# Optimization experiments

Measured on AMD Instinct MI355X. Metric: run time of the kernel, lower is better.

## Reference

```python
import jax, jax.numpy as jnp
import numpy as np

NUM_HEADS = 16


def setup_inputs() -> dict:
    key = jax.random.key(0)
    k1, k2, k3 = jax.random.split(key, 3)
    B, S, D = 4, 2048, 1024
    hidden_states = jax.random.normal(k1, (B, S, D), dtype=jnp.float32)
    w_qkv = jax.random.normal(k2, (D, 3 * D), dtype=jnp.float32) * (1.0 / np.sqrt(D))
    w_out = jax.random.normal(k3, (D, D), dtype=jnp.float32) * (1.0 / np.sqrt(D))
    return {"hidden_states": hidden_states, "w_qkv": w_qkv, "w_out": w_out}


def reference(hidden_states, w_qkv, w_out):
    B, S, D = hidden_states.shape
    H = NUM_HEADS
    d = D // H
    # fused QKV projection: [B, S, 3D] -> [3, B, S, H, d]
    qkv = (hidden_states @ w_qkv).reshape(B, S, 3, H, d)
    q, k, v = jnp.moveaxis(qkv, 2, 0)  # each [B, S, H, d]
    scale = 1.0 / np.sqrt(d).astype(np.float32)
    scores = jnp.einsum("bqhd,bkhd->bhqk", q, k) * scale  # [B, H, S, S]
    attn = jax.nn.softmax(scores, axis=-1)
    ctx = jnp.einsum("bhqk,bkhd->bqhd", attn, v).reshape(B, S, D)
    return ctx @ w_out
```

## Files before the change

kernel.cpp:

```cpp
#include <hip/hip_runtime.h>
#include <hip/hip_bf16.h>
#include <math.h>

typedef __bf16 bf16;
typedef __bf16 bf16x4 __attribute__((ext_vector_type(4)));
typedef __bf16 bf16x8 __attribute__((ext_vector_type(8)));
typedef float  f32x4  __attribute__((ext_vector_type(4)));

#define B_  4
#define S_  2048
#define D_  1024
#define H_  16
#define DH  64
#define M_  (B_*S_)
#define BH_ (B_*H_)

#define QSCALE 0.18033688011112042f

__device__ __forceinline__ void glds16(const bf16* g, bf16* l) {
  __builtin_amdgcn_global_load_lds((const __attribute__((address_space(1))) void*)g,
                                   (__attribute__((address_space(3))) void*)l, 16, 0, 0);
}

__global__ __launch_bounds__(256) void prep(const float* __restrict__ hidden, bf16* __restrict__ hb,
                                            const float* __restrict__ wqkv, const float* __restrict__ wout,
                                            bf16* __restrict__ wqkvT, bf16* __restrict__ woutT) {
  int bx = blockIdx.x, tid = threadIdx.x;
  if (bx < 8192) {
    int i = (bx * 256 + tid) * 4;
    float4 v = *(const float4*)(hidden + i);
    bf16x4 o = { (bf16)v.x, (bf16)v.y, (bf16)v.z, (bf16)v.w };
    *(bf16x4*)(hb + i) = o;
    return;
  }
  __shared__ float tile[32][33];
  int t = bx - 8192;
  const float* in; bf16* out; int C, c0, r0;
  if (t < 96 * 32) { in = wqkv; out = wqkvT; C = 3072; c0 = (t % 96) * 32; r0 = (t / 96) * 32; }
  else { t -= 96 * 32;  in = wout; out = woutT; C = 1024; c0 = (t % 32) * 32; r0 = (t / 32) * 32; }
  int tx = tid & 31, ty = tid >> 5;
  #pragma unroll
  for (int i = ty; i < 32; i += 8) tile[i][tx] = in[(size_t)(r0 + i) * C + c0 + tx];
  __syncthreads();
  #pragma unroll
  for (int i = ty; i < 32; i += 8) out[(size_t)(c0 + i) * D_ + r0 + tx] = (bf16)tile[tx][i];
}

#define BM 256
#define BN 128
#define BK 64
#define NTILE (D_ / BK)
#define ATILE (BM * BK)
#define BTILE (BN * BK)

__device__ __forceinline__ void core256(const bf16* __restrict__ A, const bf16* __restrict__ Bt,
                                        int m0, int n0, bf16* As, bf16* Bs, int tid,
                                        f32x4 acc[4][4]) {
  const int wave = tid >> 6, lane = tid & 63, quad = lane >> 4, l16 = lane & 15;
  const int wm = (wave >> 1) * 64, wn = (wave & 1) * 64;
  const int lr8 = lane >> 3, lg = lane & 7;
  const int sg = ((lg ^ lr8) << 3);
  const bf16* gA = A  + (size_t)(m0 + lr8) * D_ + sg;
  const bf16* gB = Bt + (size_t)(n0 + lr8) * D_ + sg;
  const int swq  = ((quad ^ (l16 & 7)) << 3);
  const int swq4 = (((4 + quad) ^ (l16 & 7)) << 3);

#define STAGE256(slot, kt) do {                                                    \
    int koff = (kt) * BK;                                                          \
    bf16* a_d = As + (slot) * ATILE + wave * 2048;                                 \
    bf16* b_d = Bs + (slot) * BTILE + wave * 1024;                                 \
    _Pragma("unroll")                                                              \
    for (int i_ = 0; i_ < 4; i_++)                                                 \
      glds16(gA + (size_t)(wave * 32 + i_ * 8) * D_ + koff, a_d + i_ * 512);       \
    _Pragma("unroll")                                                              \
    for (int i_ = 0; i_ < 2; i_++)                                                 \
      glds16(gB + (size_t)(wave * 16 + i_ * 8) * D_ + koff, b_d + i_ * 512);       \
  } while (0)

#define RDFRAG(slot, sw, af, bfr) do {                                             \
    const bf16* a_s = As + (slot) * ATILE;                                         \
    const bf16* b_s = Bs + (slot) * BTILE;                                         \
    _Pragma("unroll")                                                              \
    for (int i_ = 0; i_ < 4; i_++) af[i_]  = *(const bf16x8*)(a_s + (wm + i_ * 16 + l16) * 64 + (sw)); \
    _Pragma("unroll")                                                              \
    for (int j_ = 0; j_ < 4; j_++) bfr[j_] = *(const bf16x8*)(b_s + (wn + j_ * 16 + l16) * 64 + (sw)); \
  } while (0)

#define MFMA16(af, bfr) do {                                                       \
    __builtin_amdgcn_s_setprio(1);                                                 \
    _Pragma("unroll")                                                              \
    for (int i_ = 0; i_ < 4; i_++)                                                 \
      _Pragma("unroll")                                                            \
      for (int j_ = 0; j_ < 4; j_++)                                               \
        acc[i_][j_] = __builtin_amdgcn_mfma_f32_16x16x32_bf16(af[i_], bfr[j_], acc[i_][j_], 0, 0, 0); \
    __builtin_amdgcn_s_setprio(0);                                                 \
  } while (0)

  STAGE256(0, 0); STAGE256(1, 1);
  asm volatile("s_waitcnt vmcnt(6)" ::: "memory");
  __builtin_amdgcn_sched_barrier(0);
  __builtin_amdgcn_s_barrier();
  __builtin_amdgcn_sched_barrier(0);

  int scur = 0, snxt = 2;
  for (int t = 0; t < NTILE; t++) {
    bf16x8 afA[4], bfA[4];
    RDFRAG(scur, swq, afA, bfA);
    if (t + 2 < NTILE) STAGE256(snxt, t + 2);
    __builtin_amdgcn_sched_barrier(0);
    __builtin_amdgcn_s_barrier();
    __builtin_amdgcn_sched_barrier(0);
    MFMA16(afA, bfA);
    bf16x8 afB[4], bfB[4];
    RDFRAG(scur, swq4, afB, bfB);
    MFMA16(afB, bfB);
    __builtin_amdgcn_sched_barrier(0);
    if (t < NTILE - 2)       asm volatile("s_waitcnt vmcnt(6)" ::: "memory");
    else if (t == NTILE - 2) asm volatile("s_waitcnt vmcnt(0)" ::: "memory");
    __builtin_amdgcn_sched_barrier(0);
    if (t < NTILE - 1) {
      __builtin_amdgcn_s_barrier();
      __builtin_amdgcn_sched_barrier(0);
    }
    scur = (scur == 2) ? 0 : scur + 1;
    snxt = (snxt == 2) ? 0 : snxt + 1;
  }
#undef STAGE256
#undef RDFRAG
#undef MFMA16
}

__global__ __launch_bounds__(512, 1) void gemm_qkv(const bf16* __restrict__ A, const bf16* __restrict__ Bt,
                                                   bf16* __restrict__ Qb, bf16* __restrict__ Kb,
                                                   bf16* __restrict__ Vtb) {
  __shared__ __attribute__((aligned(16))) bf16 As[3 * ATILE];
  __shared__ __attribute__((aligned(16))) bf16 Bs[3 * BTILE];
  int tid = threadIdx.x;
  int m0 = blockIdx.y * BM, n0 = blockIdx.x * BN;
  f32x4 acc[4][4] = {};
  core256(A, Bt, m0, n0, As, Bs, tid, acc);
  int wave = tid >> 6, lane = tid & 63, quad = lane >> 4, l16 = lane & 15;
  int wm = (wave >> 1) * 64, wn = (wave & 1) * 64;
  int which = n0 >> 10;
  if (which == 2) {
    #pragma unroll
    for (int i = 0; i < 4; i++) {
      int mb = m0 + wm + i * 16 + quad * 4;
      int b = mb >> 11, s = mb & 2047;
      #pragma unroll
      for (int j = 0; j < 4; j++) {
        int n = n0 + wn + j * 16 + l16;
        int h = (n >> 6) & 15, dd = n & 63;
        bf16x4 v4 = { (bf16)acc[i][j][0], (bf16)acc[i][j][1], (bf16)acc[i][j][2], (bf16)acc[i][j][3] };
        *(bf16x4*)(Vtb + ((size_t)(b * H_ + h) * DH + dd) * S_ + s) = v4;
      }
    }
  } else {
    bf16* dst = (which == 0) ? Qb : Kb;
    float sc = (which == 0) ? QSCALE : 1.0f;
    #pragma unroll
    for (int i = 0; i < 4; i++) {
      #pragma unroll
      for (int j = 0; j < 4; j++) {
        int n = n0 + wn + j * 16 + l16;
        int h = (n >> 6) & 15, dd = n & 63;
        #pragma unroll
        for (int r = 0; r < 4; r++) {
          int m = m0 + wm + i * 16 + quad * 4 + r;
          int b = m >> 11, s = m & 2047;
          dst[(((size_t)(b * H_ + h)) * S_ + s) * DH + dd] = (bf16)(acc[i][j][r] * sc);
        }
      }
    }
  }
}

__global__ __launch_bounds__(512, 1) void gemm_out(const bf16* __restrict__ A, const bf16* __restrict__ Bt,
                                                   float* __restrict__ C) {
  __shared__ __attribute__((aligned(16))) bf16 As[3 * ATILE];
  __shared__ __attribute__((aligned(16))) bf16 Bs[3 * BTILE];
  int tid = threadIdx.x;
  int m0 = blockIdx.x * BM, n0 = blockIdx.y * BN;
  f32x4 acc[4][4] = {};
  core256(A, Bt, m0, n0, As, Bs, tid, acc);
  int wave = tid >> 6, lane = tid & 63, quad = lane >> 4, l16 = lane & 15;
  int wm = (wave >> 1) * 64, wn = (wave & 1) * 64;
  #pragma unroll
  for (int i = 0; i < 4; i++)
    #pragma unroll
    for (int j = 0; j < 4; j++) {
      int n = n0 + wn + j * 16 + l16;
      #pragma unroll
      for (int r = 0; r < 4; r++) {
        int m = m0 + wm + i * 16 + quad * 4 + r;
        C[(size_t)m * D_ + n] = acc[i][j][r];
      }
    }
}

#define NT  (S_ / 64)

#define KVSW(row, col) (((row) * 64) + ((col) ^ (((row) & 7) << 3)))
#define PSW(row, col)  (((row) * 32) + ((col) ^ ((((row) >> 1) & 3) << 3)))

__global__ __launch_bounds__(256, 2) void attn(const bf16* __restrict__ Qb, const bf16* __restrict__ Kb,
                                               const bf16* __restrict__ Vtb, bf16* __restrict__ ctx) {
  __shared__ __attribute__((aligned(16))) bf16 Ks[2][64 * 64];
  __shared__ __attribute__((aligned(16))) bf16 Vs[2][64 * 64];
  __shared__ __attribute__((aligned(16))) bf16 Ps[4][64 * 32];
  int tid = threadIdx.x;
  int wave = tid >> 6, lane = tid & 63, quad = lane >> 4, l16 = lane & 15;
  int bh = blockIdx.x;
  int b = bh >> 4, h = bh & 15;
  int q0 = blockIdx.y * 256 + wave * 64;
  const bf16* Qp = Qb  + (size_t)bh * S_ * DH;
  const bf16* Kp = Kb  + (size_t)bh * S_ * DH;
  const bf16* Vp = Vtb + (size_t)bh * DH * S_;

  int srow = tid >> 3, scc = (tid & 7) << 3;
  int swz = KVSW(srow, scc);

  bf16x8 qf[4][2];
  #pragma unroll
  for (int nq = 0; nq < 4; nq++)
    #pragma unroll
    for (int ks = 0; ks < 2; ks++)
      qf[nq][ks] = *(const bf16x8*)(Qp + (size_t)(q0 + nq * 16 + l16) * DH + ks * 32 + quad * 8);

  bf16 one1 = (bf16)1.0f;
  bf16x8 onesf = { one1, one1, one1, one1, one1, one1, one1, one1 };

  f32x4 o[4][4] = {};
  f32x4 oden[4] = {};

  {
    bf16x8 k0a = *(const bf16x8*)(Kp + (size_t)srow * DH + scc);
    bf16x8 k0b = *(const bf16x8*)(Kp + (size_t)(32 + srow) * DH + scc);
    bf16x8 v0a = *(const bf16x8*)(Vp + (size_t)srow * S_ + scc);
    bf16x8 v0b = *(const bf16x8*)(Vp + (size_t)(32 + srow) * S_ + scc);
    *(bf16x8*)(Ks[0] + swz)             = k0a;
    *(bf16x8*)(Ks[0] + swz + 32 * 64)   = k0b;
    *(bf16x8*)(Vs[0] + swz)             = v0a;
    *(bf16x8*)(Vs[0] + swz + 32 * 64)   = v0b;
  }

  for (int kt = 0; kt < NT; kt++) {
    int cur = kt & 1;
    __syncthreads();

    bf16x8 ka, kb2, va, vb;
    if (kt + 1 < NT) {
      const bf16* Kn = Kp + (size_t)(kt + 1) * 64 * DH;
      const bf16* Vn = Vp + (size_t)(kt + 1) * 64;
      ka  = *(const bf16x8*)(Kn + (size_t)srow * DH + scc);
      kb2 = *(const bf16x8*)(Kn + (size_t)(32 + srow) * DH + scc);
      va  = *(const bf16x8*)(Vn + (size_t)srow * S_ + scc);
      vb  = *(const bf16x8*)(Vn + (size_t)(32 + srow) * S_ + scc);
    }

    bf16x8 vf[4][2];
    #pragma unroll
    for (int td = 0; td < 4; td++)
      #pragma unroll
      for (int ks = 0; ks < 2; ks++)
        vf[td][ks] = *(const bf16x8*)(Vs[cur] + KVSW(td * 16 + l16, ks * 32 + quad * 8));

    #pragma unroll
    for (int hh = 0; hh < 2; hh++) {
      #pragma unroll
      for (int kq2 = 0; kq2 < 2; kq2++) {
        int kq = hh * 2 + kq2;
        bf16x8 kfr[2];
        #pragma unroll
        for (int ks = 0; ks < 2; ks++)
          kfr[ks] = *(const bf16x8*)(Ks[cur] + KVSW(kq * 16 + l16, ks * 32 + quad * 8));
        #pragma unroll
        for (int nq = 0; nq < 4; nq++) {
          f32x4 st = {};
          st = __builtin_amdgcn_mfma_f32_16x16x32_bf16(kfr[0], qf[nq][0], st, 0, 0, 0);
          st = __builtin_amdgcn_mfma_f32_16x16x32_bf16(kfr[1], qf[nq][1], st, 0, 0, 0);
          bf16x4 pk;
          #pragma unroll
          for (int r = 0; r < 4; r++) pk[r] = (bf16)__builtin_amdgcn_exp2f(st[r]);
          *(bf16x4*)(&Ps[wave][PSW(nq * 16 + l16, kq2 * 16 + quad * 4)]) = pk;
        }
      }
      #pragma unroll
      for (int nq = 0; nq < 4; nq++) {
        bf16x8 pf = *(const bf16x8*)(&Ps[wave][PSW(nq * 16 + l16, quad * 8)]);
        oden[nq] = __builtin_amdgcn_mfma_f32_16x16x32_bf16(pf, onesf, oden[nq], 0, 0, 0);
        #pragma unroll
        for (int td = 0; td < 4; td++)
          o[nq][td] = __builtin_amdgcn_mfma_f32_16x16x32_bf16(pf, vf[td][hh], o[nq][td], 0, 0, 0);
      }
    }

    if (kt + 1 < NT) {
      int nxt = cur ^ 1;
      *(bf16x8*)(Ks[nxt] + swz)           = ka;
      *(bf16x8*)(Ks[nxt] + swz + 32 * 64) = kb2;
      *(bf16x8*)(Vs[nxt] + swz)           = va;
      *(bf16x8*)(Vs[nxt] + swz + 32 * 64) = vb;
    }
  }

  #pragma unroll
  for (int nq = 0; nq < 4; nq++) {
    #pragma unroll
    for (int r = 0; r < 4; r++) {
      float inv = 1.0f / oden[nq][r];
      int q = q0 + nq * 16 + quad * 4 + r;
      #pragma unroll
      for (int td = 0; td < 4; td++) {
        int dd = td * 16 + l16;
        ctx[((size_t)(b * S_) + q) * D_ + h * DH + dd] = (bf16)(o[nq][td][r] * inv);
      }
    }
  }
}

extern "C" void kernel_launch(void* const* d_in, const int* in_sizes, int n_in,
                              void* d_out, int out_size, void* d_ws, size_t ws_size,
                              hipStream_t stream) {
  (void)in_sizes; (void)n_in; (void)out_size; (void)ws_size;
  const float* hidden = (const float*)d_in[0];
  const float* w_qkv  = (const float*)d_in[1];
  const float* w_out  = (const float*)d_in[2];
  float* out = (float*)d_out;

  char* ws = (char*)d_ws;
  size_t off = 0;
  bf16* hb    = (bf16*)(ws + off); off += (size_t)M_ * D_ * 2;
  bf16* wqkvT = (bf16*)(ws + off); off += (size_t)3 * D_ * D_ * 2;
  bf16* woutT = (bf16*)(ws + off); off += (size_t)D_ * D_ * 2;
  bf16* Qb    = (bf16*)(ws + off); off += (size_t)M_ * D_ * 2;
  bf16* Kb    = (bf16*)(ws + off); off += (size_t)M_ * D_ * 2;
  bf16* Vtb   = (bf16*)(ws + off); off += (size_t)M_ * D_ * 2;
  bf16* ctxb  = hb;

  prep<<<8192 + 96 * 32 + 32 * 32, 256, 0, stream>>>(hidden, hb, w_qkv, w_out, wqkvT, woutT);
  gemm_qkv<<<dim3(3 * D_ / BN, M_ / BM), 512, 0, stream>>>(hb, wqkvT, Qb, Kb, Vtb);
  attn<<<dim3(BH_, S_ / 256), 256, 0, stream>>>(Qb, Kb, Vtb, ctxb);
  gemm_out<<<dim3(M_ / BM, D_ / BN), 512, 0, stream>>>(ctxb, woutT, out);
}
```

Before: 253.8 us.

## Split GEMM K-tile into two barrier-separated phases with interleaved half-stage loads

Restructures the GEMM main loop so each K-tile runs as two phases. Each phase reads its LDS fragments, issues half of the next tile's global-to-LDS loads, hits a barrier, then runs 16 MFMAs. The last two tiles are peeled out of the loop so the waitcnt conditionals disappear. The aim is to spread global loads and LDS reads more evenly across MFMA bursts and keep waves in lockstep. The cost is an extra barrier and an explicit lgkmcnt(0) wait per phase.

```diff
diff --git a/kernel.cpp b/kernel.cpp
--- a/kernel.cpp
+++ b/kernel.cpp
@@ -65,16 +65,22 @@
   const int swq  = ((quad ^ (l16 & 7)) << 3);
   const int swq4 = (((4 + quad) ^ (l16 & 7)) << 3);
 
-#define STAGE256(slot, kt) do {                                                    \
+#define STAGE_H1(slot, kt) do {                                                    \
     int koff = (kt) * BK;                                                          \
     bf16* a_d = As + (slot) * ATILE + wave * 2048;                                 \
     bf16* b_d = Bs + (slot) * BTILE + wave * 1024;                                 \
-    _Pragma("unroll")                                                              \
-    for (int i_ = 0; i_ < 4; i_++)                                                 \
-      glds16(gA + (size_t)(wave * 32 + i_ * 8) * D_ + koff, a_d + i_ * 512);       \
-    _Pragma("unroll")                                                              \
-    for (int i_ = 0; i_ < 2; i_++)                                                 \
-      glds16(gB + (size_t)(wave * 16 + i_ * 8) * D_ + koff, b_d + i_ * 512);       \
+    glds16(gA + (size_t)(wave * 32 + 0) * D_ + koff, a_d + 0 * 512);               \
+    glds16(gA + (size_t)(wave * 32 + 8) * D_ + koff, a_d + 1 * 512);               \
+    glds16(gB + (size_t)(wave * 16 + 0) * D_ + koff, b_d + 0 * 512);               \
+  } while (0)
+
+#define STAGE_H2(slot, kt) do {                                                    \
+    int koff = (kt) * BK;                                                          \
+    bf16* a_d = As + (slot) * ATILE + wave * 2048;                                 \
+    bf16* b_d = Bs + (slot) * BTILE + wave * 1024;                                 \
+    glds16(gA + (size_t)(wave * 32 + 16) * D_ + koff, a_d + 2 * 512);              \
+    glds16(gA + (size_t)(wave * 32 + 24) * D_ + koff, a_d + 3 * 512);              \
+    glds16(gB + (size_t)(wave * 16 + 8)  * D_ + koff, b_d + 1 * 512);              \
   } while (0)
 
 #define RDFRAG(slot, sw, af, bfr) do {                                             \
@@ -87,47 +93,53 @@
   } while (0)
 
 #define MFMA16(af, bfr) do {                                                       \
-    __builtin_amdgcn_s_setprio(1);                                                 \
     _Pragma("unroll")                                                              \
     for (int i_ = 0; i_ < 4; i_++)                                                 \
       _Pragma("unroll")                                                            \
       for (int j_ = 0; j_ < 4; j_++)                                               \
         acc[i_][j_] = __builtin_amdgcn_mfma_f32_16x16x32_bf16(af[i_], bfr[j_], acc[i_][j_], 0, 0, 0); \
+  } while (0)
+
+#define PHASE256(slot, sw, STG, VMW, ENDBAR) do {                                  \
+    bf16x8 af_[4], bf_[4];                                                         \
+    RDFRAG(slot, sw, af_, bf_);                                                    \
+    STG;                                                                           \
+    __builtin_amdgcn_sched_barrier(0);                                             \
+    __builtin_amdgcn_s_barrier();                                                  \
+    asm volatile("s_waitcnt lgkmcnt(0)" ::: "memory");                             \
+    __builtin_amdgcn_sched_barrier(0);                                             \
+    __builtin_amdgcn_s_setprio(1);                                                 \
+    MFMA16(af_, bf_);                                                              \
     __builtin_amdgcn_s_setprio(0);                                                 \
-  } while (0)
-
-  STAGE256(0, 0); STAGE256(1, 1);
+    __builtin_amdgcn_sched_barrier(0);                                             \
+    VMW;                                                                           \
+    if (ENDBAR) { __builtin_amdgcn_s_barrier(); __builtin_amdgcn_sched_barrier(0); } \
+  } while (0)
+
+  STAGE_H1(0, 0); STAGE_H2(0, 0); STAGE_H1(1, 1); STAGE_H2(1, 1);
   asm volatile("s_waitcnt vmcnt(6)" ::: "memory");
   __builtin_amdgcn_sched_barrier(0);
   __builtin_amdgcn_s_barrier();
   __builtin_amdgcn_sched_barrier(0);
 
   int scur = 0, snxt = 2;
-  for (int t = 0; t < NTILE; t++) {
-    bf16x8 afA[4], bfA[4];
-    RDFRAG(scur, swq, afA, bfA);
-    if (t + 2 < NTILE) STAGE256(snxt, t + 2);
-    __builtin_amdgcn_sched_barrier(0);
-    __builtin_amdgcn_s_barrier();
-    __builtin_amdgcn_sched_barrier(0);
-    MFMA16(afA, bfA);
-    bf16x8 afB[4], bfB[4];
-    RDFRAG(scur, swq4, afB, bfB);
-    MFMA16(afB, bfB);
-    __builtin_amdgcn_sched_barrier(0);
-    if (t < NTILE - 2)       asm volatile("s_waitcnt vmcnt(6)" ::: "memory");
-    else if (t == NTILE - 2) asm volatile("s_waitcnt vmcnt(0)" ::: "memory");
-    __builtin_amdgcn_sched_barrier(0);
-    if (t < NTILE - 1) {
-      __builtin_amdgcn_s_barrier();
-      __builtin_amdgcn_sched_barrier(0);
-    }
+  for (int t = 0; t < NTILE - 2; t++) {
+    PHASE256(scur, swq,  STAGE_H1(snxt, t + 2), (void)0, 1);
+    PHASE256(scur, swq4, STAGE_H2(snxt, t + 2),
+             asm volatile("s_waitcnt vmcnt(6)" ::: "memory"), 1);
     scur = (scur == 2) ? 0 : scur + 1;
     snxt = (snxt == 2) ? 0 : snxt + 1;
   }
-#undef STAGE256
+  PHASE256(scur, swq,  (void)0, (void)0, 1);
+  PHASE256(scur, swq4, (void)0, asm volatile("s_waitcnt vmcnt(0)" ::: "memory"), 1);
+  scur = (scur == 2) ? 0 : scur + 1;
+  PHASE256(scur, swq,  (void)0, (void)0, 1);
+  PHASE256(scur, swq4, (void)0, (void)0, 0);
+#undef STAGE_H1
+#undef STAGE_H2
 #undef RDFRAG
 #undef MFMA16
+#undef PHASE256
 }
 
 __global__ __launch_bounds__(512, 1) void gemm_qkv(const bf16* __restrict__ A, const bf16* __restrict__ Bt,
```

Measured after the change: 252.6 us, median of 2. No clear change (-0.5%).
